# Kernel tuning notes

Hardware: AMD Instinct MI355X
Metric: run time of the kernel (lower is better)

## Reference

```python
import jax, jax.numpy as jnp
import numpy as np

B, C, O = 16384, 128, 128


def setup_inputs() -> dict:
    key = jax.random.key(0)
    k1, k2, k3 = jax.random.split(key, 3)
    x = jax.random.normal(k1, (B, C, 3, 3), dtype=jnp.float32)
    # 9 stacked Conv2d(C, O, 3x3) weights/biases, position p = 3*r + c (row-major)
    W = jax.random.normal(k2, (9, O, C, 3, 3), dtype=jnp.float32) * 0.05
    b = jax.random.normal(k3, (9, O), dtype=jnp.float32) * 0.05
    return {"x": x, "W": W, "b": b}


def reference(x, W, b):
    Bn = x.shape[0]
    xr = x.reshape(Bn, C, 3, 3)
    # F.interpolate(scale_factor=3, mode='nearest'): each pixel replicated 3x3
    ins = jnp.repeat(jnp.repeat(xr, 3, axis=2), 3, axis=3)  # (B, C, 9, 9)
    # patch for output position (r, c) is ins[:, :, 2+r:5+r, 2+c:5+c]
    patches = jnp.stack(
        [ins[:, :, 2 + r:5 + r, 2 + c:5 + c] for r in range(3) for c in range(3)],
        axis=0,
    )  # (9, B, C, 3, 3)
    # each conv reduces its 3x3xC patch to one pixel per out-channel
    out = jnp.einsum('pbcij,pocij->bpo', patches, W) + b[None]  # (B, 9, O)
    out = out.transpose(0, 2, 1).reshape(Bn, O, 3, 3)  # row-major (r, c)
    return out
```

## Files before the change

kernel.cpp:

```cpp
#include <hip/hip_runtime.h>
#include <hip/hip_bf16.h>

typedef __bf16 bf16_t;
typedef __attribute__((ext_vector_type(8))) __bf16 bf16x8;
typedef __attribute__((ext_vector_type(4))) float f32x4;

#define KDIM 1152
#define NDIM 1152
#define BM 128
#define BN 192
#define BK 32
#define NIT 36
#define NTILES 6
#define A_STEP 8192
#define A_PANEL 294912
#define B_STEP 12288
#define B_TILE (36 * B_STEP)

__device__ __forceinline__ void gload_lds16(const void* g, void* l) {
    __builtin_amdgcn_global_load_lds(
        (const __attribute__((address_space(1))) void*)g,
        (__attribute__((address_space(3))) void*)l, 16, 0, 0);
}

__global__ void cvt_x(const float* __restrict__ X, bf16_t* __restrict__ Xb)
{
    const int u = blockIdx.x * 256 + threadIdx.x;
    const int w = u >> 9;
    const int P = w / 36;
    const int T = w - P * 36;
    const int rem = u & 511;
    const int rb = rem >> 6;
    const int g = (rem >> 4) & 3;
    const int r0 = rem & 15;
    const int m = P * 128 + rb * 16 + r0;
    const int k = T * 32 + g * 8;
    const float* src = X + (size_t)m * KDIM + k;
    f32x4 lo = *(const f32x4*)src;
    f32x4 hi = *(const f32x4*)(src + 4);
    bf16x8 v;
    #pragma unroll
    for (int e = 0; e < 4; ++e) { v[e] = (__bf16)lo[e]; v[4 + e] = (__bf16)hi[e]; }
    *(bf16x8*)((char*)Xb + (size_t)u * 16) = v;
}

__global__ void build_wb(const float* __restrict__ W,
                         const float* __restrict__ bvec,
                         bf16_t* __restrict__ Bm,
                         float* __restrict__ bias)
{
    const int t = blockIdx.x * blockDim.x + threadIdx.x;
    if (t < NDIM) {
        const int o = t / 9, p = t - o * 9;
        bias[t] = bvec[p * 128 + o];
    }
    const int c = t & 127;
    const int o = (t >> 7) & 127;
    const int p = t >> 14;
    if (p >= 9) return;
    const int r = p / 3, cc = p - r * 3;
    float eff[3][3] = {{0.f,0.f,0.f},{0.f,0.f,0.f},{0.f,0.f,0.f}};
    const float* w = W + (size_t)((p * 128 + o) * 128 + c) * 9;
    #pragma unroll
    for (int i = 0; i < 3; ++i) {
        const int a = (2 + r + i) / 3;
        #pragma unroll
        for (int j = 0; j < 3; ++j) {
            const int bb = (2 + cc + j) / 3;
            eff[a][bb] += w[i * 3 + j];
        }
    }
    const int n = o * 9 + p;
    const int tile = n / BN;
    const int nin = n - tile * BN;
    #pragma unroll
    for (int a = 0; a < 3; ++a)
        #pragma unroll
        for (int bb = 0; bb < 3; ++bb) {
            const int k = c * 9 + a * 3 + bb;
            const size_t idx = (size_t)tile * (B_TILE / 2)
                             + (k >> 5) * (B_STEP / 2)
                             + (nin >> 4) * 512 + ((k >> 3) & 3) * 128
                             + (nin & 15) * 8 + (k & 7);
            Bm[idx] = (bf16_t)eff[a][bb];
        }
}

__launch_bounds__(256, 3)
__global__ void ind_gemm(const bf16_t* __restrict__ Xb,
                         const bf16_t* __restrict__ Bm,
                         const float* __restrict__ bias,
                         float* __restrict__ out)
{
    __shared__ char Bs[2][B_STEP];

    const int tid = threadIdx.x;
    const int lane = tid & 63;
    const int wid = tid >> 6;
    const int wm = wid >> 1;
    const int wn = wid & 1;

    const int bid = blockIdx.x;
    const int swz = (bid & 7) * 96 + (bid >> 3);
    const int mt = swz / NTILES;
    const int nt = swz - mt * NTILES;
    const int m0 = mt * BM;

    const int fr = (lane >> 4) * 256 + (lane & 15) * 16;
    const char* apl = (const char*)Xb + (size_t)mt * A_PANEL + wm * 4096 + fr;
    const char* bpanel = (const char*)Bm + (size_t)nt * B_TILE;

    f32x4 acc[4][6];
    #pragma unroll
    for (int i = 0; i < 4; ++i)
        #pragma unroll
        for (int j = 0; j < 6; ++j)
            acc[i][j] = (f32x4){0.f, 0.f, 0.f, 0.f};

    f32x4 afA[4], afB[4];

    #define LOADA(T, AF) do {                                               \
        const char* p_ = apl + (size_t)(T) * A_STEP;                        \
        asm volatile("global_load_dwordx4 %0, %4, off\n\t"                  \
                     "global_load_dwordx4 %1, %4, off offset:1024\n\t"      \
                     "global_load_dwordx4 %2, %4, off offset:2048\n\t"      \
                     "global_load_dwordx4 %3, %4, off offset:3072"          \
                     : "=&v"(AF[0]), "=&v"(AF[1]), "=&v"(AF[2]), "=&v"(AF[3]) \
                     : "v"(p_) : "memory");                                 \
    } while (0)

    #define GLDB(T, BUF) do {                                               \
        const char* s_ = bpanel + (size_t)(T) * B_STEP;                     \
        _Pragma("unroll")                                                   \
        for (int r_ = 0; r_ < 3; ++r_) {                                    \
            const int u_ = (tid + r_ * 256) * 16;                           \
            gload_lds16(s_ + u_, &Bs[BUF][u_]);                             \
        } } while (0)

    #define MFMA24(AF) do {                                                 \
        __builtin_amdgcn_s_setprio(1);                                      \
        _Pragma("unroll")                                                   \
        for (int mi = 0; mi < 4; ++mi) {                                    \
            const bf16x8 a_ = __builtin_bit_cast(bf16x8, AF[mi]);           \
            _Pragma("unroll")                                               \
            for (int j_ = 0; j_ < 6; ++j_)                                  \
                acc[mi][j_] = __builtin_amdgcn_mfma_f32_16x16x32_bf16(      \
                    a_, bfr[j_], acc[mi][j_], 0, 0, 0);                     \
        }                                                                   \
        __builtin_amdgcn_s_setprio(0);                                      \
    } while (0)

    #define RDB(CUR) do {                                                   \
        _Pragma("unroll")                                                   \
        for (int j_ = 0; j_ < 6; ++j_)                                      \
            bfr[j_] = *(const bf16x8*)(&Bs[CUR][(wn * 6 + j_) * 1024 + fr]); \
        asm volatile("s_waitcnt lgkmcnt(0)" ::: "memory");                  \
        __builtin_amdgcn_sched_barrier(0);                                  \
        __builtin_amdgcn_s_barrier();                                       \
    } while (0)

    bf16x8 bfr[6];

    LOADA(0, afA);
    GLDB(0, 0);
    GLDB(1, 1);
    asm volatile("s_waitcnt vmcnt(3)" ::: "memory");
    __builtin_amdgcn_sched_barrier(0);
    __builtin_amdgcn_s_barrier();

    #pragma unroll 1
    for (int t2 = 0; t2 < 17; ++t2) {
        const int t = 2 * t2;
        RDB(0);
        LOADA(t + 1, afB);
        GLDB(t + 2, 0);
        MFMA24(afA);
        asm volatile("s_waitcnt vmcnt(3)" ::: "memory");
        __builtin_amdgcn_sched_barrier(0);
        __builtin_amdgcn_s_barrier();
        RDB(1);
        LOADA(t + 2, afA);
        GLDB(t + 3, 1);
        MFMA24(afB);
        asm volatile("s_waitcnt vmcnt(3)" ::: "memory");
        __builtin_amdgcn_sched_barrier(0);
        __builtin_amdgcn_s_barrier();
    }
    RDB(0);
    LOADA(35, afB);
    MFMA24(afA);
    asm volatile("s_waitcnt vmcnt(0)" ::: "memory");
    __builtin_amdgcn_sched_barrier(0);
    __builtin_amdgcn_s_barrier();
    {
        #pragma unroll
        for (int j_ = 0; j_ < 6; ++j_)
            bfr[j_] = *(const bf16x8*)(&Bs[1][(wn * 6 + j_) * 1024 + fr]);
        asm volatile("s_waitcnt lgkmcnt(0)" ::: "memory");
        __builtin_amdgcn_sched_barrier(0);
        MFMA24(afB);
    }

    #undef LOADA
    #undef GLDB
    #undef MFMA24
    #undef RDB

    const int orow = (lane >> 4) * 4;
    const int ocol = lane & 15;
    const int gn0 = nt * BN + wn * 96 + ocol;
    #pragma unroll
    for (int ni = 0; ni < 6; ++ni) {
        const float bv = bias[gn0 + ni * 16];
        #pragma unroll
        for (int mi = 0; mi < 4; ++mi) {
            float* po = out + (size_t)(m0 + wm * 64 + mi * 16 + orow) * NDIM
                            + gn0 + ni * 16;
            #pragma unroll
            for (int r = 0; r < 4; ++r)
                po[(size_t)r * NDIM] = acc[mi][ni][r] + bv;
        }
    }
}

extern "C" void kernel_launch(void* const* d_in, const int* in_sizes, int n_in,
                              void* d_out, int out_size, void* d_ws, size_t ws_size,
                              hipStream_t stream)
{
    const float* x  = (const float*)d_in[0];
    const float* W  = (const float*)d_in[1];
    const float* bv = (const float*)d_in[2];
    float* out = (float*)d_out;

    bf16_t* Xb   = (bf16_t*)d_ws;
    bf16_t* Bm   = (bf16_t*)((char*)d_ws + (size_t)16384 * KDIM * sizeof(bf16_t));
    float*  bias = (float*)((char*)Bm + (size_t)KDIM * NDIM * sizeof(bf16_t));

    cvt_x<<<9216, 256, 0, stream>>>(x, Xb);
    build_wb<<<576, 256, 0, stream>>>(W, bv, Bm, bias);
    ind_gemm<<<768, 256, 0, stream>>>(Xb, Bm, bias, out);
}
```

Baseline: 90.53 us.

## Merge prep kernels, coalesce X conversion reads via LDS, deepen A-fragment prefetch

The two preprocessing kernels are merged into one launch: the first blocks convert X to bf16 and the rest build the weight matrix and bias. The X conversion now has each group of four lanes read contiguous row segments and transposes them through LDS before writing, which makes the global reads coalesced. In the GEMM main loop the A fragment for the next-next step is now issued after the MFMAs, giving two steps of prefetch, with the vmcnt waits adjusted to match. This adds register pressure and a block barrier in the conversion path in exchange for fewer launches and more latency hiding.

After: 80.77 us. -10.8%, faster.

```diff
diff --git a/kernel.cpp b/kernel.cpp
--- a/kernel.cpp
+++ b/kernel.cpp
@@ -16,6 +16,7 @@
 #define A_PANEL 294912
 #define B_STEP 12288
 #define B_TILE (36 * B_STEP)
+#define CVT_BLOCKS 9216
 
 __device__ __forceinline__ void gload_lds16(const void* g, void* l) {
     __builtin_amdgcn_global_load_lds(
@@ -23,33 +24,36 @@
         (__attribute__((address_space(3))) void*)l, 16, 0, 0);
 }
 
-__global__ void cvt_x(const float* __restrict__ X, bf16_t* __restrict__ Xb)
+__global__ void prep(const float* __restrict__ X, bf16_t* __restrict__ Xb,
+                     const float* __restrict__ W, const float* __restrict__ bvec,
+                     bf16_t* __restrict__ Bm, float* __restrict__ bias)
 {
-    const int u = blockIdx.x * 256 + threadIdx.x;
-    const int w = u >> 9;
-    const int P = w / 36;
-    const int T = w - P * 36;
-    const int rem = u & 511;
-    const int rb = rem >> 6;
-    const int g = (rem >> 4) & 3;
-    const int r0 = rem & 15;
-    const int m = P * 128 + rb * 16 + r0;
-    const int k = T * 32 + g * 8;
-    const float* src = X + (size_t)m * KDIM + k;
-    f32x4 lo = *(const f32x4*)src;
-    f32x4 hi = *(const f32x4*)(src + 4);
-    bf16x8 v;
-    #pragma unroll
-    for (int e = 0; e < 4; ++e) { v[e] = (__bf16)lo[e]; v[4 + e] = (__bf16)hi[e]; }
-    *(bf16x8*)((char*)Xb + (size_t)u * 16) = v;
-}
-
-__global__ void build_wb(const float* __restrict__ W,
-                         const float* __restrict__ bvec,
-                         bf16_t* __restrict__ Bm,
-                         float* __restrict__ bias)
-{
-    const int t = blockIdx.x * blockDim.x + threadIdx.x;
+    __shared__ char L[4096];
+    const int bid = blockIdx.x;
+    const int tid = threadIdx.x;
+    if (bid < CVT_BLOCKS) {
+        const int wv = (bid << 2) + (tid >> 6);
+        const int l = tid & 63;
+        const int P = wv / 288;
+        const int rem = wv - P * 288;
+        const int T = rem >> 3;
+        const int rb = rem & 7;
+        const int row = P * 128 + rb * 16 + (l >> 2);
+        const int k = T * 32 + (l & 3) * 8;
+        const float* src = X + (size_t)row * KDIM + k;
+        f32x4 lo = *(const f32x4*)src;
+        f32x4 hi = *(const f32x4*)(src + 4);
+        bf16x8 v;
+        #pragma unroll
+        for (int e = 0; e < 4; ++e) { v[e] = (__bf16)lo[e]; v[4 + e] = (__bf16)hi[e]; }
+        char* wl = L + (tid >> 6) * 1024;
+        *(bf16x8*)(wl + ((l & 3) * 16 + (l >> 2)) * 16) = v;
+        __builtin_amdgcn_s_barrier();
+        bf16x8 o = *(const bf16x8*)(wl + l * 16);
+        *(bf16x8*)((char*)Xb + ((size_t)wv * 64 + l) * 16) = o;
+        return;
+    }
+    const int t = (bid - CVT_BLOCKS) * 256 + tid;
     if (t < NDIM) {
         const int o = t / 9, p = t - o * 9;
         bias[t] = bvec[p * 128 + o];
@@ -118,6 +122,7 @@
             acc[i][j] = (f32x4){0.f, 0.f, 0.f, 0.f};
 
     f32x4 afA[4], afB[4];
+    bf16x8 bfr[6];
 
     #define LOADA(T, AF) do {                                               \
         const char* p_ = apl + (size_t)(T) * A_STEP;                        \
@@ -136,6 +141,15 @@
             const int u_ = (tid + r_ * 256) * 16;                           \
             gload_lds16(s_ + u_, &Bs[BUF][u_]);                             \
         } } while (0)
+
+    #define RDB(CUR) do {                                                   \
+        _Pragma("unroll")                                                   \
+        for (int j_ = 0; j_ < 6; ++j_)                                      \
+            bfr[j_] = *(const bf16x8*)(&Bs[CUR][(wn * 6 + j_) * 1024 + fr]); \
+        asm volatile("s_waitcnt lgkmcnt(0)" ::: "memory");                  \
+        __builtin_amdgcn_sched_barrier(0);                                  \
+        __builtin_amdgcn_s_barrier();                                       \
+    } while (0)
 
     #define MFMA24(AF) do {                                                 \
         __builtin_amdgcn_s_setprio(1);                                      \
@@ -150,61 +164,46 @@
         __builtin_amdgcn_s_setprio(0);                                      \
     } while (0)
 
-    #define RDB(CUR) do {                                                   \
-        _Pragma("unroll")                                                   \
-        for (int j_ = 0; j_ < 6; ++j_)                                      \
-            bfr[j_] = *(const bf16x8*)(&Bs[CUR][(wn * 6 + j_) * 1024 + fr]); \
-        asm volatile("s_waitcnt lgkmcnt(0)" ::: "memory");                  \
+    #define WAITV(N) do {                                                   \
+        asm volatile("s_waitcnt vmcnt(" #N ")" ::: "memory");               \
         __builtin_amdgcn_sched_barrier(0);                                  \
-        __builtin_amdgcn_s_barrier();                                       \
-    } while (0)
-
-    bf16x8 bfr[6];
+    } while (0)
 
     LOADA(0, afA);
     GLDB(0, 0);
+    LOADA(1, afB);
     GLDB(1, 1);
-    asm volatile("s_waitcnt vmcnt(3)" ::: "memory");
-    __builtin_amdgcn_sched_barrier(0);
+    WAITV(7);
     __builtin_amdgcn_s_barrier();
 
     #pragma unroll 1
     for (int t2 = 0; t2 < 17; ++t2) {
         const int t = 2 * t2;
         RDB(0);
-        LOADA(t + 1, afB);
         GLDB(t + 2, 0);
         MFMA24(afA);
-        asm volatile("s_waitcnt vmcnt(3)" ::: "memory");
-        __builtin_amdgcn_sched_barrier(0);
+        LOADA(t + 2, afA);
+        WAITV(7);
         __builtin_amdgcn_s_barrier();
         RDB(1);
-        LOADA(t + 2, afA);
         GLDB(t + 3, 1);
         MFMA24(afB);
-        asm volatile("s_waitcnt vmcnt(3)" ::: "memory");
-        __builtin_amdgcn_sched_barrier(0);
+        LOADA(t + 3, afB);
+        WAITV(7);
         __builtin_amdgcn_s_barrier();
     }
     RDB(0);
-    LOADA(35, afB);
     MFMA24(afA);
-    asm volatile("s_waitcnt vmcnt(0)" ::: "memory");
-    __builtin_amdgcn_sched_barrier(0);
+    WAITV(0);
     __builtin_amdgcn_s_barrier();
-    {
-        #pragma unroll
-        for (int j_ = 0; j_ < 6; ++j_)
-            bfr[j_] = *(const bf16x8*)(&Bs[1][(wn * 6 + j_) * 1024 + fr]);
-        asm volatile("s_waitcnt lgkmcnt(0)" ::: "memory");
-        __builtin_amdgcn_sched_barrier(0);
-        MFMA24(afB);
-    }
+    RDB(1);
+    MFMA24(afB);
 
     #undef LOADA
     #undef GLDB
+    #undef RDB
     #undef MFMA24
-    #undef RDB
+    #undef WAITV
 
     const int orow = (lane >> 4) * 4;
     const int ocol = lane & 15;
@@ -236,7 +235,6 @@
     bf16_t* Bm   = (bf16_t*)((char*)d_ws + (size_t)16384 * KDIM * sizeof(bf16_t));
     float*  bias = (float*)((char*)Bm + (size_t)KDIM * NDIM * sizeof(bf16_t));
 
-    cvt_x<<<9216, 256, 0, stream>>>(x, Xb);
-    build_wb<<<576, 256, 0, stream>>>(W, bv, Bm, bias);
+    prep<<<CVT_BLOCKS + 576, 256, 0, stream>>>(x, Xb, W, bv, Bm, bias);
     ind_gemm<<<768, 256, 0, stream>>>(Xb, Bm, bias, out);
 }
```
